# Kernel optimization log

Hardware: AMD Instinct MI355X
Metric: run time of the kernel (lower is better)

Reference implementation:

```python
import jax, jax.numpy as jnp
import numpy as np

# Module hyperparameters (init_kwargs)
NH = 254          # nHidden
NSTEP = 32        # MPC horizon
DT = 1.0 / 60.0   # del_t
EPS = 1e-4
PQ = 5.0
QV = 200.0
QA = 1.0
N_STATE = NH + 2  # hidden embedding + [position, velocity]
NBATCH = 256


def setup_inputs() -> dict:
    key = jax.random.key(0)
    k1, k2, k3, k4, k5, k6 = jax.random.split(key, 6)
    x = jax.random.normal(k1, (NBATCH, NH), dtype=jnp.float32)
    gripper_p = jax.random.normal(k2, (NBATCH,), dtype=jnp.float32)
    own_gripper_v = jax.random.normal(k3, (NBATCH,), dtype=jnp.float32)
    other_gripper_v = jax.random.normal(k4, (NBATCH,), dtype=jnp.float32)
    # Learned parameters (as in __init__): Af ~ U[0,1), Lq = tril(U[0,1))
    Af = jax.random.uniform(k5, (NH, 1), dtype=jnp.float32)
    Lq = jnp.tril(jax.random.uniform(k6, (NH, NH), dtype=jnp.float32))
    return {"x": x, "gripper_p": gripper_p, "own_gripper_v": own_gripper_v,
            "other_gripper_v": other_gripper_v, "Af": Af, "Lq": Lq}


def _mpc_forward(x, gripper_p, own_gripper_v, Af, Lq):
    n = N_STATE
    dt = x.dtype
    eye_n = jnp.eye(n, dtype=dt)

    # ---- Q0: [[Lq Lq^T + eps I, 0], [0, diag(0, Qv)]]  (n x n) ----
    Q0_tl = Lq @ Lq.T + EPS * jnp.eye(NH, dtype=dt)
    Q0 = jnp.zeros((n, n), dt).at[:NH, :NH].set(Q0_tl).at[NH + 1, NH + 1].set(QV)
    w = jnp.ones((NSTEP,), dt).at[-1].set(PQ)        # final-step weight Pq
    Q0_stack = w[:, None, None] * Q0                 # [NSTEP, n, n]
    Q_dia = jax.scipy.linalg.block_diag(*Q0_stack)   # [NSTEP*n, NSTEP*n]

    # ---- A0: [[I, 0, Af], [0, 1, dt], [0, 0, 1]] ----
    A0 = jnp.zeros((n, n), dt)
    A0 = A0.at[:NH, :NH].set(jnp.eye(NH, dtype=dt)).at[:NH, NH + 1].set(Af[:, 0])
    A0 = A0.at[NH, NH].set(1.0).at[NH, NH + 1].set(DT).at[NH + 1, NH + 1].set(1.0)

    # ---- powers A0^1..A0^NSTEP via scan (replaces the Python power loop) ----
    def step(carry, _):
        nxt = carry @ A0
        return nxt, nxt
    _, Pk = jax.lax.scan(step, eye_n, None, length=NSTEP)   # Pk[k] = A0^{k+1}
    P = jnp.concatenate([eye_n[None], Pk], axis=0)          # A0^0 .. A0^NSTEP
    T_ = Pk.reshape(NSTEP * n, n)                           # vstack(A0^1..A0^NSTEP)

    # ---- AN_: block lower-triangular Toeplitz, block (i,j) = A0^{i-j} for j<=i ----
    d = jnp.arange(NSTEP)[:, None] - jnp.arange(NSTEP)[None, :]
    blocks = jnp.where((d >= 0)[:, :, None, None],
                       P[jnp.clip(d, 0, NSTEP)], jnp.zeros((), dt))  # [NSTEP,NSTEP,n,n]
    AN_ = blocks.transpose(0, 2, 1, 3).reshape(NSTEP * n, NSTEP * n)

    B0 = jnp.zeros((n, 1), dt).at[NH, 0].set(0.5 * DT * DT).at[NH + 1, 0].set(DT)
    B_dia = jax.scipy.linalg.block_diag(*jnp.broadcast_to(B0, (NSTEP, n, 1)))

    S_ = AN_ @ B_dia                                        # [NSTEP*n, NSTEP]
    QS = Q_dia @ S_                                         # [NSTEP*n, NSTEP]
    Q_final = 2.0 * (QA * jnp.eye(NSTEP, dtype=dt) + S_.T @ QS) \
              + EPS * jnp.eye(NSTEP, dtype=dt)
    p_final = 2.0 * (T_.T @ QS)                             # [n, NSTEP]

    # ---- batch state x0 = [x, gripper_p, own_gripper_v] ----
    x0 = jnp.concatenate([x, gripper_p[:, None], own_gripper_v[:, None]], axis=1)
    p_x0 = x0 @ p_final                                     # [B, NSTEP]

    # QPFunction with G=0, h=0, no equalities -> unconstrained QP:
    # u = argmin 0.5 u^T Q_final u + p_x0^T u = -Q_final^{-1} p_x0
    u = -jnp.linalg.solve(Q_final, p_x0.T).T                # [B, NSTEP]

    # x_predict = S u + T x0 ; output picks position component (index NH) per step
    x_pred = u @ S_.T + x0 @ T_.T                           # [B, NSTEP*n]
    posi = x_pred.reshape(-1, NSTEP, n)[:, :, NH]           # [B, NSTEP]
    return posi


def reference(x, gripper_p, own_gripper_v, other_gripper_v, Af, Lq):
    # other_gripper_v is accepted but unused in the active forward path (as in source)
    return _mpc_forward(x, gripper_p, own_gripper_v, Af, Lq)
```

## Files before the change

### kernel.cpp

```cpp
#include <hip/hip_runtime.h>

#define NH 254
#define NSTEP 32
#define NB 256

constexpr float  FEPS = 1e-4f;
constexpr double DDT  = 1.0 / 60.0;
constexpr double DQV  = 200.0;
constexpr double DPQ  = 5.0;
constexpr double DQA  = 1.0;
constexpr double DEPS = 1e-4;

__global__ __launch_bounds__(1024) void k_mono(const float* __restrict__ Lq,
                                               const float* __restrict__ Af,
                                               const float* __restrict__ x,
                                               const float* __restrict__ gp,
                                               const float* __restrict__ gv,
                                               float* __restrict__ out) {
    __shared__ float  af_sh[256];
    __shared__ float  tpart[4][256];
    __shared__ float  t_sh[256];
    __shared__ float  g_sh[256];
    __shared__ double red[4];
    __shared__ double M[32][34];
    __shared__ double ua[32], ub[32];
    __shared__ float  cA[32], cB[32];

    const int tid  = threadIdx.x;
    const int k8   = tid & 255;
    const int q    = tid >> 8;
    const int lane = tid & 63;
    const int wv   = tid >> 6;

    if (q == 0) af_sh[k8] = (k8 < NH) ? Af[k8] : 0.f;
    if (tid == 0) { g_sh[254] = 0.f; g_sh[255] = 0.f; }
    __syncthreads();

    {
        float acc = 0.f;
        const int ibase = q * 64;
        if (k8 < NH && k8 < ibase + 64) {
            const int iend = (ibase + 64 < NH) ? ibase + 64 : NH;
            for (int i0 = ibase; i0 < iend; i0 += 8) {
                float v[8];
                #pragma unroll
                for (int j = 0; j < 8; ++j)
                    v[j] = (i0 + j < iend) ? Lq[(i0 + j) * NH + k8] : 0.f;
                #pragma unroll
                for (int j = 0; j < 8; ++j)
                    acc += v[j] * af_sh[i0 + j];
            }
        }
        tpart[q][k8] = acc;
    }
    __syncthreads();
    if (tid < 256)
        t_sh[tid] = tpart[0][tid] + tpart[1][tid] + tpart[2][tid] + tpart[3][tid];
    __syncthreads();

    for (int r = 0; r < 16; r += 2) {
        const int i1 = wv + 16 * r;
        const int i2 = i1 + 16;
        float lv1[4], lv2[4];
        #pragma unroll
        for (int c = 0; c < 4; ++c) {
            const int kk = lane + 64 * c;
            lv1[c] = (kk <= i1) ? Lq[i1 * NH + kk] : 0.f;
            lv2[c] = (i2 < NH && kk <= i2) ? Lq[i2 * NH + kk] : 0.f;
        }
        float a1 = 0.f, a2 = 0.f;
        #pragma unroll
        for (int c = 0; c < 4; ++c) {
            const int kk = lane + 64 * c;
            a1 += lv1[c] * t_sh[kk];
            a2 += lv2[c] * t_sh[kk];
        }
        #pragma unroll
        for (int off = 32; off; off >>= 1) {
            a1 += __shfl_xor(a1, off, 64);
            a2 += __shfl_xor(a2, off, 64);
        }
        if (lane == 0) {
            g_sh[i1] = a1 + FEPS * af_sh[i1];
            if (i2 < NH) g_sh[i2] = a2 + FEPS * af_sh[i2];
        }
    }
    __syncthreads();

    {
        double dv = 0.0;
        if (tid < NH) {
            const double td = (double)t_sh[tid];
            const double ad = (double)af_sh[tid];
            dv = td * td + DEPS * ad * ad;
        }
        #pragma unroll
        for (int off = 32; off; off >>= 1) dv += __shfl_xor(dv, off, 64);
        if (wv < 4 && lane == 0) red[wv] = dv;
    }
    __syncthreads();
    const double c = red[0] + red[1] + red[2] + red[3];

    {
        const int j1 = tid >> 5, j2 = tid & 31;
        const int m = (j1 > j2) ? j1 : j2;
        double s = 0.0;
        for (int kk = m; kk < 32; ++kk) {
            const double wk = (kk == 31) ? DPQ : 1.0;
            s += wk * ((double)(kk - j1) * (double)(kk - j2) * c + DQV);
        }
        M[j1][j2] = 2.0 * DDT * DDT * s + ((j1 == j2) ? (2.0 * DQA + DEPS) : 0.0);
    }
    if (tid < 32) {
        const int j = tid;
        double sa = 0.0, sb = 0.0;
        for (int kk = j; kk < 32; ++kk) {
            const double wk = (kk == 31) ? DPQ : 1.0;
            sa += wk * (double)(kk - j);
            sb += wk * ((double)(kk + 1) * (double)(kk - j) * c + DQV);
        }
        M[j][32] = 2.0 * DDT * sa;
        M[j][33] = 2.0 * DDT * sb;
    }
    __syncthreads();

    {
        const int r  = tid & 31;
        const int cg = tid >> 5;
        for (int p = 0; p < 32; ++p) {
            const double f = M[r][p] / M[p][p];
            if (r != p) {
                if (cg > p) M[r][cg] -= f * M[p][cg];
                const int c2 = cg + 32;
                if (c2 < 34) M[r][c2] -= f * M[p][c2];
            }
            __syncthreads();
        }
    }
    if (tid < 32) {
        ua[tid] = -M[tid][32] / M[tid][tid];
        ub[tid] = -M[tid][33] / M[tid][tid];
    }
    __syncthreads();
    if (tid < 32) {
        const int i = tid;
        double ca = 0.0, cb = 0.0;
        for (int j = 0; j <= i; ++j) {
            const double wgt = (double)(i - j) + 0.5;
            ca += wgt * ua[j];
            cb += wgt * ub[j];
        }
        cA[i] = (float)(ca * DDT * DDT);
        cB[i] = (float)((double)(i + 1) * DDT + cb * DDT * DDT);
    }
    __syncthreads();

    for (int r = 0; r < 16; r += 2) {
        const int b1 = wv + 16 * r;
        const int b2 = b1 + 16;
        float xa[4], xb[4];
        #pragma unroll
        for (int cidx = 0; cidx < 4; ++cidx) {
            const int kk = lane + 64 * cidx;
            xa[cidx] = (kk < NH) ? x[b1 * NH + kk] : 0.f;
            xb[cidx] = (kk < NH) ? x[b2 * NH + kk] : 0.f;
        }
        float s1 = 0.f, s2 = 0.f;
        #pragma unroll
        for (int cidx = 0; cidx < 4; ++cidx) {
            const int kk = lane + 64 * cidx;
            s1 += xa[cidx] * g_sh[kk];
            s2 += xb[cidx] * g_sh[kk];
        }
        #pragma unroll
        for (int off = 32; off; off >>= 1) {
            s1 += __shfl_xor(s1, off, 64);
            s2 += __shfl_xor(s2, off, 64);
        }
        if (lane < 32) {
            out[b1 * NSTEP + lane] = gp[b1] + gv[b1] * cB[lane] + s1 * cA[lane];
            out[b2 * NSTEP + lane] = gp[b2] + gv[b2] * cB[lane] + s2 * cA[lane];
        }
    }
}

extern "C" void kernel_launch(void* const* d_in, const int* in_sizes, int n_in,
                              void* d_out, int out_size, void* d_ws, size_t ws_size,
                              hipStream_t stream) {
    const float* x  = (const float*)d_in[0];
    const float* gp = (const float*)d_in[1];
    const float* gv = (const float*)d_in[2];
    const float* Af = (const float*)d_in[4];
    const float* Lq = (const float*)d_in[5];
    float* out = (float*)d_out;

    k_mono<<<1, 1024, 0, stream>>>(Lq, Af, x, gp, gv, out);
}
```

Before: 93.16 us.

## Split into per-batch blocks with redundant solve and fused projection

Launches one 256-thread block per batch row instead of a single 1024-thread block. Each block recomputes the Lq-derived vectors and the 32x32 solve redundantly, then fuses the x·g dot product directly into its output. This spreads the work across many compute units and removes the serial batch loop, but every block now rereads all of Lq and repeats the elimination with fewer threads.

```diff
diff --git a/kernel.cpp b/kernel.cpp
--- a/kernel.cpp
+++ b/kernel.cpp
@@ -11,81 +11,80 @@
 constexpr double DQA  = 1.0;
 constexpr double DEPS = 1e-4;
 
-__global__ __launch_bounds__(1024) void k_mono(const float* __restrict__ Lq,
+__global__ __launch_bounds__(256) void k_fused(const float* __restrict__ Lq,
                                                const float* __restrict__ Af,
                                                const float* __restrict__ x,
                                                const float* __restrict__ gp,
                                                const float* __restrict__ gv,
                                                float* __restrict__ out) {
     __shared__ float  af_sh[256];
-    __shared__ float  tpart[4][256];
+    __shared__ float  x_sh[256];
     __shared__ float  t_sh[256];
-    __shared__ float  g_sh[256];
+    __shared__ float  svals[4];
     __shared__ double red[4];
     __shared__ double M[32][34];
     __shared__ double ua[32], ub[32];
     __shared__ float  cA[32], cB[32];
 
+    const int b    = blockIdx.x;
     const int tid  = threadIdx.x;
-    const int k8   = tid & 255;
-    const int q    = tid >> 8;
     const int lane = tid & 63;
     const int wv   = tid >> 6;
 
-    if (q == 0) af_sh[k8] = (k8 < NH) ? Af[k8] : 0.f;
-    if (tid == 0) { g_sh[254] = 0.f; g_sh[255] = 0.f; }
+    const float gpv = gp[b];
+    const float gvv = gv[b];
+
+    af_sh[tid] = (tid < NH) ? Af[tid] : 0.f;
+    x_sh[tid]  = (tid < NH) ? x[b * NH + tid] : 0.f;
     __syncthreads();
 
     {
         float acc = 0.f;
-        const int ibase = q * 64;
-        if (k8 < NH && k8 < ibase + 64) {
-            const int iend = (ibase + 64 < NH) ? ibase + 64 : NH;
-            for (int i0 = ibase; i0 < iend; i0 += 8) {
-                float v[8];
+        if (tid < NH) {
+            for (int i0 = (tid & ~31); i0 < NH; i0 += 32) {
+                float v[32];
                 #pragma unroll
-                for (int j = 0; j < 8; ++j)
-                    v[j] = (i0 + j < iend) ? Lq[(i0 + j) * NH + k8] : 0.f;
+                for (int j = 0; j < 32; ++j) {
+                    const int i = i0 + j;
+                    v[j] = (i < NH) ? Lq[i * NH + tid] : 0.f;
+                }
                 #pragma unroll
-                for (int j = 0; j < 8; ++j)
+                for (int j = 0; j < 32; ++j)
                     acc += v[j] * af_sh[i0 + j];
             }
         }
-        tpart[q][k8] = acc;
+        t_sh[tid] = acc;
     }
     __syncthreads();
-    if (tid < 256)
-        t_sh[tid] = tpart[0][tid] + tpart[1][tid] + tpart[2][tid] + tpart[3][tid];
-    __syncthreads();
 
-    for (int r = 0; r < 16; r += 2) {
-        const int i1 = wv + 16 * r;
-        const int i2 = i1 + 16;
-        float lv1[4], lv2[4];
-        #pragma unroll
-        for (int c = 0; c < 4; ++c) {
-            const int kk = lane + 64 * c;
-            lv1[c] = (kk <= i1) ? Lq[i1 * NH + kk] : 0.f;
-            lv2[c] = (i2 < NH && kk <= i2) ? Lq[i2 * NH + kk] : 0.f;
+    {
+        float sacc = 0.f;
+        for (int r = 0; r < 64; r += 4) {
+            float a4[4] = {0.f, 0.f, 0.f, 0.f};
+            #pragma unroll
+            for (int rr = 0; rr < 4; ++rr) {
+                const int i = 64 * wv + r + rr;
+                #pragma unroll
+                for (int c = 0; c < 4; ++c) {
+                    const int kk = lane + 64 * c;
+                    const float lv = (i < NH && kk < NH) ? Lq[i * NH + kk] : 0.f;
+                    a4[rr] += lv * t_sh[kk];
+                }
+            }
+            #pragma unroll
+            for (int rr = 0; rr < 4; ++rr) {
+                #pragma unroll
+                for (int off = 32; off; off >>= 1)
+                    a4[rr] += __shfl_xor(a4[rr], off, 64);
+            }
+            #pragma unroll
+            for (int rr = 0; rr < 4; ++rr) {
+                const int i = 64 * wv + r + rr;
+                sacc += x_sh[i] * (a4[rr] + FEPS * af_sh[i]);
+            }
         }
-        float a1 = 0.f, a2 = 0.f;
-        #pragma unroll
-        for (int c = 0; c < 4; ++c) {
-            const int kk = lane + 64 * c;
-            a1 += lv1[c] * t_sh[kk];
-            a2 += lv2[c] * t_sh[kk];
-        }
-        #pragma unroll
-        for (int off = 32; off; off >>= 1) {
-            a1 += __shfl_xor(a1, off, 64);
-            a2 += __shfl_xor(a2, off, 64);
-        }
-        if (lane == 0) {
-            g_sh[i1] = a1 + FEPS * af_sh[i1];
-            if (i2 < NH) g_sh[i2] = a2 + FEPS * af_sh[i2];
-        }
+        if (lane == 0) svals[wv] = sacc;
     }
-    __syncthreads();
 
     {
         double dv = 0.0;
@@ -96,13 +95,13 @@
         }
         #pragma unroll
         for (int off = 32; off; off >>= 1) dv += __shfl_xor(dv, off, 64);
-        if (wv < 4 && lane == 0) red[wv] = dv;
+        if (lane == 0) red[wv] = dv;
     }
     __syncthreads();
     const double c = red[0] + red[1] + red[2] + red[3];
 
-    {
-        const int j1 = tid >> 5, j2 = tid & 31;
+    for (int e = tid; e < 1024; e += 256) {
+        const int j1 = e >> 5, j2 = e & 31;
         const int m = (j1 > j2) ? j1 : j2;
         double s = 0.0;
         for (int kk = m; kk < 32; ++kk) {
@@ -125,14 +124,13 @@
     __syncthreads();
 
     {
-        const int r  = tid & 31;
-        const int cg = tid >> 5;
+        const int r   = tid & 31;
+        const int cg8 = tid >> 5;
         for (int p = 0; p < 32; ++p) {
             const double f = M[r][p] / M[p][p];
             if (r != p) {
-                if (cg > p) M[r][cg] -= f * M[p][cg];
-                const int c2 = cg + 32;
-                if (c2 < 34) M[r][c2] -= f * M[p][c2];
+                for (int cc = cg8; cc < 34; cc += 8)
+                    if (cc > p) M[r][cc] -= f * M[p][cc];
             }
             __syncthreads();
         }
@@ -155,32 +153,9 @@
     }
     __syncthreads();
 
-    for (int r = 0; r < 16; r += 2) {
-        const int b1 = wv + 16 * r;
-        const int b2 = b1 + 16;
-        float xa[4], xb[4];
-        #pragma unroll
-        for (int cidx = 0; cidx < 4; ++cidx) {
-            const int kk = lane + 64 * cidx;
-            xa[cidx] = (kk < NH) ? x[b1 * NH + kk] : 0.f;
-            xb[cidx] = (kk < NH) ? x[b2 * NH + kk] : 0.f;
-        }
-        float s1 = 0.f, s2 = 0.f;
-        #pragma unroll
-        for (int cidx = 0; cidx < 4; ++cidx) {
-            const int kk = lane + 64 * cidx;
-            s1 += xa[cidx] * g_sh[kk];
-            s2 += xb[cidx] * g_sh[kk];
-        }
-        #pragma unroll
-        for (int off = 32; off; off >>= 1) {
-            s1 += __shfl_xor(s1, off, 64);
-            s2 += __shfl_xor(s2, off, 64);
-        }
-        if (lane < 32) {
-            out[b1 * NSTEP + lane] = gp[b1] + gv[b1] * cB[lane] + s1 * cA[lane];
-            out[b2 * NSTEP + lane] = gp[b2] + gv[b2] * cB[lane] + s2 * cA[lane];
-        }
+    if (tid < 32) {
+        const float s = svals[0] + svals[1] + svals[2] + svals[3];
+        out[b * NSTEP + tid] = gpv + gvv * cB[tid] + s * cA[tid];
     }
 }
 
@@ -194,5 +169,5 @@
     const float* Lq = (const float*)d_in[5];
     float* out = (float*)d_out;
 
-    k_mono<<<1, 1024, 0, stream>>>(Lq, Af, x, gp, gv, out);
+    k_fused<<<NB, 256, 0, stream>>>(Lq, Af, x, gp, gv, out);
 }
```

Measured after the change: 106.8 us. 14.6% more time.
